# Kernel tuning notes

Measured on AMD Instinct MI355X. Metric: run time of the kernel, lower is better.

Reference implementation:

```python
import jax, jax.numpy as jnp
import numpy as np

N_NODES = 100000
N_EDGES = 1200000
IN_CH = 128
HID = 256
OUT_CH = 64
N_ETYPES = 8
N_DIFF = 1000


def setup_inputs() -> dict:
    key = jax.random.key(0)
    ks = jax.random.split(key, 20)
    s = 0.05
    inp = {
        'x': jax.random.normal(ks[0], (N_NODES, IN_CH), jnp.float32),
        'edge_index': jax.random.randint(ks[1], (2, N_EDGES), 0, N_NODES, jnp.int64),
        'edge_type': jax.random.randint(ks[2], (N_EDGES,), 0, N_ETYPES, jnp.int64),
        'diff_idx': jax.random.randint(ks[3], (N_DIFF,), 0, N_NODES, jnp.int64),
        # lin: in_ch -> hid -> out_ch
        'lin1_w': jax.random.normal(ks[4], (HID, IN_CH), jnp.float32) * s,
        'lin1_b': jnp.zeros((HID,), jnp.float32),
        'lin2_w': jax.random.normal(ks[5], (OUT_CH, HID), jnp.float32) * s,
        'lin2_b': jnp.zeros((OUT_CH,), jnp.float32),
        # GRUCell(out_ch, out_ch): gates ordered r, z, n as in torch
        'gru_w_ih': jax.random.normal(ks[6], (3 * OUT_CH, OUT_CH), jnp.float32) * s,
        'gru_w_hh': jax.random.normal(ks[7], (3 * OUT_CH, OUT_CH), jnp.float32) * s,
        'gru_b_ih': jnp.zeros((3 * OUT_CH,), jnp.float32),
        'gru_b_hh': jnp.zeros((3 * OUT_CH,), jnp.float32),
        'edge_type_weight': jax.random.normal(ks[8], (N_ETYPES,), jnp.float32),
        # fc: out_ch -> hid -> 2
        'fc1_w': jax.random.normal(ks[9], (HID, OUT_CH), jnp.float32) * s,
        'fc1_b': jnp.zeros((HID,), jnp.float32),
        'fc2_w': jax.random.normal(ks[10], (2, HID), jnp.float32) * s,
        'fc2_b': jnp.zeros((2,), jnp.float32),
        'w_imp': jnp.float32(1.0),
    }
    return inp


def _gru_cell(m, h, w_ih, w_hh, b_ih, b_hh):
    # torch GRUCell: gates [r, z, n]
    gi = m @ w_ih.T + b_ih  # [N, 3H]
    gh = h @ w_hh.T + b_hh
    gi_r, gi_z, gi_n = jnp.split(gi, 3, axis=-1)
    gh_r, gh_z, gh_n = jnp.split(gh, 3, axis=-1)
    r = jax.nn.sigmoid(gi_r + gh_r)
    z = jax.nn.sigmoid(gi_z + gh_z)
    n = jnp.tanh(gi_n + r * gh_n)
    return (1.0 - z) * n + z * h


def reference(x, edge_index, edge_type, diff_idx,
              lin1_w, lin1_b, lin2_w, lin2_b,
              gru_w_ih, gru_w_hh, gru_b_ih, gru_b_hh,
              edge_type_weight,
              fc1_w, fc1_b, fc2_w, fc2_b, w_imp):
    N = x.shape[0]
    src, dst = edge_index[0], edge_index[1]
    # input projection MLP
    h = jax.nn.relu(x @ lin1_w.T + lin1_b) @ lin2_w.T + lin2_b  # [N, OUT]
    # per-edge softplus weight (constant across iterations)
    w_e = jax.nn.softplus(edge_type_weight[edge_type])[:, None]  # [E, 1]
    # degree for mean aggregation (isolated nodes -> 0 message)
    deg = jax.ops.segment_sum(jnp.ones_like(src, dtype=h.dtype), dst, num_segments=N)
    deg = jnp.maximum(deg, 1.0)[:, None]
    for _ in range(3):
        msg = w_e * h[src]  # gather + weight, [E, OUT]
        m = jax.ops.segment_sum(msg, dst, num_segments=N) / deg  # scatter-mean
        h = _gru_cell(m, h, gru_w_ih, gru_w_hh, gru_b_ih, gru_b_hh)
    # importance-weighted global pooling
    w_pos = jax.nn.softplus(w_imp)
    alpha = jnp.ones((N, 1), h.dtype).at[diff_idx].set(1.0 + w_pos)
    pooled = (alpha * h).sum(axis=0, keepdims=True) / alpha.sum()  # [1, OUT]
    out = jax.nn.relu(pooled @ fc1_w.T + fc1_b) @ fc2_w.T + fc2_b  # [1, 2]
    return jax.nn.log_softmax(out, axis=1)
```

## Files before the change

kernel.cpp:

```cpp
#include <hip/hip_runtime.h>
#include <math.h>

#define NN 100000
#define NE 1200000
#define NDIFF 1000
#define CAP 48
#define SLICE 2048
#define NQ 200
#define SUBN 500
#define QCAPB 32
#define NSH 8
#define SQS 1024
#define NSPLAY 32
#define PSTRIDE 132

typedef short short8 __attribute__((ext_vector_type(8)));
typedef float floatx4 __attribute__((ext_vector_type(4)));
typedef float floatx2 __attribute__((ext_vector_type(2)));
typedef unsigned short ushort_t;
typedef unsigned long long ull_t;

__device__ __forceinline__ float softplusf_(float x) {
  return fmaxf(x, 0.f) + logf(1.f + __expf(-fabsf(x)));
}
__device__ __forceinline__ float sigmoidf_(float x) {
  return 1.f / (1.f + __expf(-x));
}
__device__ __forceinline__ float tanhf_fast(float x) {
  float ax = fabsf(x);
  float e = __expf(-2.f * ax);
  float t = (1.f - e) / (1.f + e);
  return x < 0.f ? -t : t;
}
__device__ __forceinline__ ushort_t f2bf(float f) {
  unsigned u = __float_as_uint(f);
  unsigned r = (u + 0x7FFFu + ((u >> 16) & 1u)) >> 16;
  return (ushort_t)r;
}
__device__ __forceinline__ float bf2f(ushort_t s) {
  return __uint_as_float(((unsigned)s) << 16);
}
__device__ __forceinline__ uint2 bf8_to_fp8x8(short8 v) {
  float f[8];
  #pragma unroll
  for (int i = 0; i < 8; ++i) f[i] = bf2f((ushort_t)v[i]);
  int a = 0, b = 0;
  a = __builtin_amdgcn_cvt_pk_fp8_f32(f[0], f[1], a, false);
  a = __builtin_amdgcn_cvt_pk_fp8_f32(f[2], f[3], a, true);
  b = __builtin_amdgcn_cvt_pk_fp8_f32(f[4], f[5], b, false);
  b = __builtin_amdgcn_cvt_pk_fp8_f32(f[6], f[7], b, true);
  uint2 r; r.x = (unsigned)a; r.y = (unsigned)b;
  return r;
}


__global__ void prep_w_kernel(const float* __restrict__ lin1_w, const float* __restrict__ lin2_w,
                              const float* __restrict__ w_ih, const float* __restrict__ w_hh,
                              const float* __restrict__ etw, const int* __restrict__ diff,
                              ushort_t* __restrict__ W1s, ushort_t* __restrict__ W2s,
                              ushort_t* __restrict__ Wcs, float* __restrict__ wtab,
                              unsigned char* __restrict__ flagb) {
  int i = blockIdx.x * 256 + threadIdx.x;
  if (i < 8) wtab[i] = softplusf_(etw[i]);
  if (i < NDIFF) flagb[diff[i]] = 1;
  if (i < 32768) {
    int fi = i >> 9, lane = (i >> 3) & 63, j = i & 7;
    int s = fi >> 4, ct = fi & 15;
    int quad = lane >> 4, l15 = lane & 15;
    int col = ct * 16 + l15, k = s * 32 + quad * 8 + j;
    W1s[i] = f2bf(lin1_w[col * 128 + k]);
  } else if (i < 49152) {
    int i2 = i - 32768;
    int fi = i2 >> 9, lane = (i2 >> 3) & 63, j = i2 & 7;
    int s = fi >> 2, ct = fi & 3;
    int quad = lane >> 4, l15 = lane & 15;
    int col = ct * 16 + l15, k = s * 32 + quad * 8 + j;
    W2s[i2] = f2bf(lin2_w[col * 256 + k]);
  } else {
    int i3 = i - 49152;
    int fi = i3 >> 9, lane = (i3 >> 3) & 63, j = i3 & 7;
    int s = fi >> 4, ct = fi & 15;
    int quad = lane >> 4, l15 = lane & 15;
    int jj = ct * 16 + l15, k = s * 32 + quad * 8 + j;
    float v;
    if (jj < 128)      v = (k < 64) ? w_ih[jj * 64 + k] : w_hh[jj * 64 + (k - 64)];
    else if (jj < 192) v = (k < 64) ? w_ih[jj * 64 + k] : 0.f;
    else               v = (k < 64) ? 0.f : w_hh[(jj - 64) * 64 + (k - 64)];
    Wcs[i3] = f2bf(v);
  }
}


__launch_bounds__(256)
__global__ void bin_kernel(const int* __restrict__ src, const int* __restrict__ dst,
                           const int* __restrict__ etype,
                           unsigned* __restrict__ gtail, ull_t* __restrict__ staging) {
  __shared__ uint2 bin[NQ][QCAPB];
  __shared__ unsigned lcur[NQ];
  int t = threadIdx.x;
  int shard = blockIdx.x & 7;
  for (int i = t; i < NQ; i += 256) lcur[i] = 0;
  __syncthreads();
  int base = blockIdx.x * SLICE;

  uint2 rec[8];
  int qq[8];
  unsigned idx[8];
  #pragma unroll
  for (int it = 0; it < 8; ++it) {
    int e = base + it * 256 + t;
    qq[it] = -1;
    if (e < NE) {
      int d = __builtin_nontemporal_load(&dst[e]);
      int s = __builtin_nontemporal_load(&src[e]);
      int tv = __builtin_nontemporal_load(&etype[e]);
      rec[it].x = (unsigned)(s | (tv << 17));
      rec[it].y = (unsigned)d;
      int q = d / SUBN;
      qq[it] = q;
      unsigned i = atomicAdd(&lcur[q], 1u);
      idx[it] = i;
      if (i < QCAPB) bin[q][i] = rec[it];
    }
  }
  __syncthreads();
  if (t < NQ) {
    unsigned c = min(lcur[t], (unsigned)QCAPB);
    if (c) {
      unsigned gb = atomicAdd(&gtail[(t * NSH + shard) * 16], c);
      ull_t* qst = staging + (size_t)(t * NSH + shard) * SQS + gb;
      const uint2* b = bin[t];
      for (unsigned i = 0; i < c; ++i)
        qst[i] = ((ull_t)b[i].y << 32) | (ull_t)b[i].x;
    }
  }
  #pragma unroll
  for (int it = 0; it < 8; ++it) {
    if (qq[it] >= 0 && idx[it] >= QCAPB) {
      unsigned gb = atomicAdd(&gtail[(qq[it] * NSH + shard) * 16], 1u);
      staging[(size_t)(qq[it] * NSH + shard) * SQS + gb] =
          ((ull_t)rec[it].y << 32) | (ull_t)rec[it].x;
    }
  }
}

__launch_bounds__(512)
__global__ void scatter_kernel(const ull_t* __restrict__ staging,
                               const unsigned* __restrict__ gtail,
                               unsigned* __restrict__ cpack, int* __restrict__ csr) {
  __shared__ int cnt[SUBN];
  int t = threadIdx.x;
  int q = blockIdx.x;
  int n0 = q * SUBN;
  for (int i = t; i < SUBN; i += 512) cnt[i] = 0;
  __syncthreads();

  #pragma unroll 1
  for (int sh = 0; sh < NSH; ++sh) {
    unsigned n = gtail[(q * NSH + sh) * 16];
    const ull_t* st = staging + (size_t)(q * NSH + sh) * SQS;
    for (unsigned i = t; i < n; i += 512) {
      ull_t r = st[i];
      int d = (int)(r >> 32);
      int rank = atomicAdd(&cnt[d - n0], 1);
      csr[d * CAP + rank] = (int)(unsigned)r;
    }
  }
  __syncthreads();

  if (t < SUBN / 4) {
    unsigned w = (unsigned)cnt[t * 4] | ((unsigned)cnt[t * 4 + 1] << 8) |
                 ((unsigned)cnt[t * 4 + 2] << 16) | ((unsigned)cnt[t * 4 + 3] << 24);
    cpack[(n0 >> 2) + t] = w;
  }
}


__launch_bounds__(256)
__global__ void mlp_kernel(const float* __restrict__ x,
                           const ushort_t* __restrict__ W1s, const float* __restrict__ b1,
                           const ushort_t* __restrict__ W2s, const float* __restrict__ b2,
                           ushort_t* __restrict__ mh, unsigned char* __restrict__ h8) {
  __shared__ ushort_t S[64 * 264];
  int t = threadIdx.x;
  int wv = t >> 6, lane = t & 63;
  int quad = lane >> 4, l15 = lane & 15;
  int nb = blockIdx.x * 64;

  #pragma unroll
  for (int it = 0; it < 8; ++it) {
    int f = it * 256 + t;
    int row = f >> 5, off4 = f & 31;
    int grow = min(nb + row, NN - 1);
    float4 v = *(const float4*)&x[(size_t)grow * 128 + off4 * 4];
    union { uint2 d; ushort_t u[4]; } pk;
    pk.u[0] = f2bf(v.x); pk.u[1] = f2bf(v.y); pk.u[2] = f2bf(v.z); pk.u[3] = f2bf(v.w);
    *(uint2*)&S[row * 136 + off4 * 4] = pk.d;
  }
  __syncthreads();

  floatx4 acc1[4][4];
  #pragma unroll
  for (int rt = 0; rt < 4; ++rt)
    #pragma unroll
    for (int c = 0; c < 4; ++c) acc1[rt][c] = (floatx4)0.f;

  #pragma unroll
  for (int s = 0; s < 4; ++s) {
    short8 av[4];
    #pragma unroll
    for (int rt = 0; rt < 4; ++rt)
      av[rt] = *(const short8*)&S[(rt * 16 + l15) * 136 + s * 32 + quad * 8];
    #pragma unroll
    for (int c = 0; c < 4; ++c) {
      short8 bv = *(const short8*)&W1s[((s * 16 + wv * 4 + c) * 64 + lane) * 8];
      #pragma unroll
      for (int rt = 0; rt < 4; ++rt)
        acc1[rt][c] = __builtin_amdgcn_mfma_f32_16x16x32_bf16(av[rt], bv, acc1[rt][c], 0, 0, 0);
    }
  }
  __syncthreads();

  #pragma unroll
  for (int c = 0; c < 4; ++c) {
    int col = (wv * 4 + c) * 16 + l15;
    float bb = b1[col];
    #pragma unroll
    for (int rt = 0; rt < 4; ++rt)
      #pragma unroll
      for (int reg = 0; reg < 4; ++reg)
        S[(rt * 16 + quad * 4 + reg) * 264 + col] = f2bf(fmaxf(acc1[rt][c][reg] + bb, 0.f));
  }
  __syncthreads();

  floatx4 acc2[4];
  #pragma unroll
  for (int c = 0; c < 4; ++c) acc2[c] = (floatx4)0.f;
  #pragma unroll
  for (int s = 0; s < 8; ++s) {
    short8 av = *(const short8*)&S[(wv * 16 + l15) * 264 + s * 32 + quad * 8];
    #pragma unroll
    for (int c = 0; c < 4; ++c) {
      short8 bv = *(const short8*)&W2s[((s * 4 + c) * 64 + lane) * 8];
      acc2[c] = __builtin_amdgcn_mfma_f32_16x16x32_bf16(av, bv, acc2[c], 0, 0, 0);
    }
  }
  __syncthreads();

  #pragma unroll
  for (int c = 0; c < 4; ++c) {
    int col = c * 16 + l15;
    float bb = b2[c * 16 + l15];
    #pragma unroll
    for (int reg = 0; reg < 4; ++reg)
      S[(wv * 16 + quad * 4 + reg) * 72 + col] = f2bf(acc2[c][reg] + bb);
  }
  __syncthreads();

  #pragma unroll
  for (int it = 0; it < 2; ++it) {
    int idx = it * 256 + t;
    int row = idx >> 3, ch = idx & 7;
    int node = nb + row;
    if (node < NN) {
      short8 v = *(const short8*)&S[row * 72 + ch * 8];
      *(short8*)&mh[(size_t)node * 64 + ch * 8] = v;
      *(uint2*)&h8[(size_t)node * 64 + ch * 8] = bf8_to_fp8x8(v);
    }
  }
}


template <bool LAST>
__launch_bounds__(256, 8)
__global__ void agru_kernel(const ushort_t* __restrict__ mhin,
                            const unsigned char* __restrict__ h8in,
                            const unsigned* __restrict__ cpack,
                            const int* __restrict__ csr, const float* __restrict__ wtab,
                            const ushort_t* __restrict__ Wcs,
                            const float* __restrict__ b_ih, const float* __restrict__ b_hh,
                            ushort_t* __restrict__ mhout, unsigned char* __restrict__ h8out,
                            const unsigned char* __restrict__ flagb,
                            float* __restrict__ pooled) {
  __shared__ ushort_t As[32 * 136];
  __shared__ ushort_t Os[32 * 72];
  __shared__ float wt[16];
  __shared__ float red[132];
  int t = threadIdx.x;
  int nb = blockIdx.x * 32;
  if (t < 16) wt[t] = (t < 8) ? wtab[t] : 0.f;
  if (LAST) { for (int i = t; i < 132; i += 256) red[i] = 0.f; }
  __syncthreads();

  int g8 = t >> 3, lane8 = t & 7;
  int node = nb + g8;

  short8 hreg = *(const short8*)&mhin[(size_t)node * 64 + lane8 * 8];

  int deg = (cpack[node >> 2] >> ((node & 3) * 8)) & 255;
  int s = node * CAP;
  float f0 = 0.f, f1 = 0.f, f2 = 0.f, f3 = 0.f;
  float f4 = 0.f, f5 = 0.f, f6 = 0.f, f7 = 0.f;
  for (int p = 0; p < deg; p += 8) {
    int k[8];
    uint2 v[8];
    #pragma unroll
    for (int i = 0; i < 8; ++i) {
      int q = p + i;
      k[i] = (q < deg) ? __builtin_nontemporal_load(&csr[s + q]) : (8 << 17);
    }
    #pragma unroll
    for (int i = 0; i < 8; ++i)
      v[i] = *(const uint2*)&h8in[(size_t)(k[i] & 0x1FFFF) * 64 + lane8 * 8];
    #pragma unroll
    for (int i = 0; i < 8; ++i) {
      float w = wt[k[i] >> 17];
      floatx2 xlo = __builtin_amdgcn_cvt_pk_f32_fp8((int)v[i].x, false);
      floatx2 xhi = __builtin_amdgcn_cvt_pk_f32_fp8((int)v[i].x, true);
      floatx2 ylo = __builtin_amdgcn_cvt_pk_f32_fp8((int)v[i].y, false);
      floatx2 yhi = __builtin_amdgcn_cvt_pk_f32_fp8((int)v[i].y, true);
      f0 += w * xlo[0]; f1 += w * xlo[1]; f2 += w * xhi[0]; f3 += w * xhi[1];
      f4 += w * ylo[0]; f5 += w * ylo[1]; f6 += w * yhi[0]; f7 += w * yhi[1];
    }
  }
  {
    float invd = 1.f / fmaxf((float)deg, 1.f);
    short8 pk;
    pk[0] = (short)f2bf(f0 * invd); pk[1] = (short)f2bf(f1 * invd);
    pk[2] = (short)f2bf(f2 * invd); pk[3] = (short)f2bf(f3 * invd);
    pk[4] = (short)f2bf(f4 * invd); pk[5] = (short)f2bf(f5 * invd);
    pk[6] = (short)f2bf(f6 * invd); pk[7] = (short)f2bf(f7 * invd);
    *(short8*)&As[g8 * 136 + lane8 * 8] = pk;
    *(short8*)&As[g8 * 136 + 64 + lane8 * 8] = hreg;
  }
  __syncthreads();

  int wv = t >> 6, lane = t & 63;
  int quad = lane >> 4, l15 = lane & 15;

  floatx4 acc[2][4];
  #pragma unroll
  for (int rt = 0; rt < 2; ++rt)
    #pragma unroll
    for (int g = 0; g < 4; ++g) acc[rt][g] = (floatx4)0.f;

  #pragma unroll
  for (int s4 = 0; s4 < 4; ++s4) {
    short8 av[2];
    #pragma unroll
    for (int rt = 0; rt < 2; ++rt)
      av[rt] = *(const short8*)&As[(rt * 16 + l15) * 136 + s4 * 32 + quad * 8];
    #pragma unroll
    for (int g = 0; g < 4; ++g) {
      short8 bv = *(const short8*)&Wcs[((s4 * 16 + g * 4 + wv) * 64 + lane) * 8];
      #pragma unroll
      for (int rt = 0; rt < 2; ++rt)
        acc[rt][g] = __builtin_amdgcn_mfma_f32_16x16x32_bf16(av[rt], bv, acc[rt][g], 0, 0, 0);
    }
  }

  int j = wv * 16 + l15;
  float bir = b_ih[j] + b_hh[j];
  float biz = b_ih[64 + j] + b_hh[64 + j];
  float bin_ = b_ih[128 + j];
  float bhn = b_hh[128 + j];

  if (!LAST) {
    #pragma unroll
    for (int rt = 0; rt < 2; ++rt) {
      #pragma unroll
      for (int reg = 0; reg < 4; ++reg) {
        int lrow = rt * 16 + quad * 4 + reg;
        float r = sigmoidf_(acc[rt][0][reg] + bir);
        float z = sigmoidf_(acc[rt][1][reg] + biz);
        float n = tanhf_fast(acc[rt][2][reg] + bin_ + r * (acc[rt][3][reg] + bhn));
        float hp = bf2f(As[lrow * 136 + 64 + j]);
        Os[lrow * 72 + j] = f2bf((1.f - z) * n + z * hp);
      }
    }
    __syncthreads();
    short8 vo = *(const short8*)&Os[g8 * 72 + lane8 * 8];
    *(short8*)&mhout[(size_t)node * 64 + lane8 * 8] = vo;
    *(uint2*)&h8out[(size_t)node * 64 + lane8 * 8] = bf8_to_fp8x8(vo);
  } else {
    float psum = 0.f, fsum = 0.f;
    #pragma unroll
    for (int rt = 0; rt < 2; ++rt) {
      #pragma unroll
      for (int reg = 0; reg < 4; ++reg) {
        int lrow = rt * 16 + quad * 4 + reg;
        float r = sigmoidf_(acc[rt][0][reg] + bir);
        float z = sigmoidf_(acc[rt][1][reg] + biz);
        float n = tanhf_fast(acc[rt][2][reg] + bin_ + r * (acc[rt][3][reg] + bhn));
        float hp = bf2f(As[lrow * 136 + 64 + j]);
        float hn = (1.f - z) * n + z * hp;
        psum += hn;
        if (flagb[nb + lrow]) fsum += hn;
      }
    }
    atomicAdd(&red[j], psum);
    atomicAdd(&red[64 + j], fsum);
    if (t < 32) { if (flagb[nb + t]) atomicAdd(&red[128], 1.f); }
    __syncthreads();
    if (t < 129) atomicAdd(&pooled[(blockIdx.x & (NSPLAY - 1)) * PSTRIDE + t], red[t]);
  }
}


__global__ void final_kernel(const float* __restrict__ pooled,
                             const float* __restrict__ fc1_w, const float* __restrict__ fc1_b,
                             const float* __restrict__ fc2_w, const float* __restrict__ fc2_b,
                             const float* __restrict__ w_imp, float* __restrict__ out) {
  __shared__ float p[64];
  __shared__ float hid[256];
  __shared__ float o[2];
  __shared__ float cnt_s;
  int t = threadIdx.x;
  float wpos = softplusf_(w_imp[0]);
  float b = 0.f, f = 0.f;
  if (t < 64) {
    #pragma unroll 4
    for (int k = 0; k < NSPLAY; ++k) {
      b += pooled[k * PSTRIDE + t];
      f += pooled[k * PSTRIDE + 64 + t];
    }
  }
  if (t == 64) {
    float c = 0.f;
    for (int k = 0; k < NSPLAY; ++k) c += pooled[k * PSTRIDE + 128];
    cnt_s = c;
  }
  __syncthreads();
  if (t < 64) {
    float den = (float)NN + wpos * cnt_s;
    p[t] = (b + wpos * f) / den;
  }
  __syncthreads();
  {
    float a = 0.f;
    for (int k = 0; k < 64; ++k) a += p[k] * fc1_w[t * 64 + k];
    hid[t] = fmaxf(a + fc1_b[t], 0.f);
  }
  __syncthreads();
  if (t < 2) {
    float a = 0.f;
    for (int k = 0; k < 256; ++k) a += hid[k] * fc2_w[t * 256 + k];
    o[t] = a + fc2_b[t];
  }
  __syncthreads();
  if (t == 0) {
    float mx = fmaxf(o[0], o[1]);
    float lse = mx + logf(__expf(o[0] - mx) + __expf(o[1] - mx));
    out[0] = o[0] - lse;
    out[1] = o[1] - lse;
  }
}


extern "C" void kernel_launch(void* const* d_in, const int* in_sizes, int n_in,
                              void* d_out, int out_size, void* d_ws, size_t ws_size,
                              hipStream_t stream) {
  const float* x        = (const float*)d_in[0];
  const int*   ei       = (const int*)d_in[1];
  const int*   etype    = (const int*)d_in[2];
  const int*   diff_idx = (const int*)d_in[3];
  const float* lin1_w   = (const float*)d_in[4];
  const float* lin1_b   = (const float*)d_in[5];
  const float* lin2_w   = (const float*)d_in[6];
  const float* lin2_b   = (const float*)d_in[7];
  const float* gru_w_ih = (const float*)d_in[8];
  const float* gru_w_hh = (const float*)d_in[9];
  const float* gru_b_ih = (const float*)d_in[10];
  const float* gru_b_hh = (const float*)d_in[11];
  const float* etw      = (const float*)d_in[12];
  const float* fc1_w    = (const float*)d_in[13];
  const float* fc1_b    = (const float*)d_in[14];
  const float* fc2_w    = (const float*)d_in[15];
  const float* fc2_b    = (const float*)d_in[16];
  const float* w_imp    = (const float*)d_in[17];
  float* out = (float*)d_out;

  char* ws = (char*)d_ws;
  size_t off = 0;
  auto alloc = [&](size_t bytes) -> void* {
    void* p = ws + off;
    off += (bytes + 255) & ~(size_t)255;
    return p;
  };
  ushort_t* mh0   = (ushort_t*)alloc((size_t)NN * 64 * 2);
  ushort_t* mh1   = (ushort_t*)alloc((size_t)NN * 64 * 2);
  unsigned char* h8a = (unsigned char*)alloc((size_t)NN * 64);
  unsigned char* h8b = (unsigned char*)alloc((size_t)NN * 64);
  int*   csr      = (int*)  alloc((size_t)NN * CAP * 4);
  ull_t* staging  = (ull_t*)alloc((size_t)NQ * NSH * SQS * 8);
  ushort_t* W1s   = (ushort_t*)alloc(128 * 256 * 2);
  ushort_t* W2s   = (ushort_t*)alloc(256 * 64 * 2);
  ushort_t* Wcs   = (ushort_t*)alloc(128 * 256 * 2);
  float* wtab     = (float*)alloc(8 * 4);
  const size_t gtb = (size_t)NQ * NSH * 16 * 4;
  const size_t plb = (size_t)NSPLAY * PSTRIDE * 4;
  char* zbase     = (char*)alloc(gtb + (size_t)NN + NN + plb);
  unsigned* gtail = (unsigned*)zbase;
  unsigned* cpack = (unsigned*)(zbase + gtb);
  unsigned char* flagb = (unsigned char*)(zbase + gtb + NN);
  float* pooled   = (float*)(zbase + gtb + NN + NN);
  const size_t zbytes = gtb + (size_t)NN + NN + plb;

  const int ngemm = (NN + 63) / 64;
  const int nagru = NN / 32;
  const int nbin  = (NE + SLICE - 1) / SLICE;

  hipMemsetAsync(zbase, 0, zbytes, stream);
  prep_w_kernel<<<320, 256, 0, stream>>>(lin1_w, lin2_w, gru_w_ih, gru_w_hh, etw, diff_idx,
                                         W1s, W2s, Wcs, wtab, flagb);
  bin_kernel<<<nbin, 256, 0, stream>>>(ei, ei + NE, etype, gtail, staging);
  scatter_kernel<<<NQ, 512, 0, stream>>>(staging, gtail, cpack, csr);
  mlp_kernel<<<ngemm, 256, 0, stream>>>(x, W1s, lin1_b, W2s, lin2_b, mh0, h8a);

  agru_kernel<false><<<nagru, 256, 0, stream>>>(mh0, h8a, cpack, csr, wtab, Wcs,
                                                gru_b_ih, gru_b_hh, mh1, h8b, flagb, pooled);
  agru_kernel<false><<<nagru, 256, 0, stream>>>(mh1, h8b, cpack, csr, wtab, Wcs,
                                                gru_b_ih, gru_b_hh, mh0, h8a, flagb, pooled);
  agru_kernel<true><<<nagru, 256, 0, stream>>>(mh0, h8a, cpack, csr, wtab, Wcs,
                                               gru_b_ih, gru_b_hh, mh1, h8b, flagb, pooled);

  final_kernel<<<1, 256, 0, stream>>>(pooled, fc1_w, fc1_b, fc2_w, fc2_b, w_imp, out);
}
```

Before: 322.6 us.

## Fuse edge binning with input MLP and pack staging records into 32 bits

Merges the edge-binning kernel and the input-projection MLP kernel into one launch, with block ranges split by blockIdx, so the two independent phases can run concurrently and one launch is saved. Staging records shrink from 64-bit to 32-bit by storing the node's local offset within its partition instead of the full destination, which halves staging traffic. The aggregation loop now reads CSR indices as 16-byte vectors, 12 per iteration instead of 8 scalar loads, with extra padding on the CSR allocation. Risks are shared-memory and occupancy changes in the fused kernel and reads past the degree in the vector loads.

```diff
diff --git a/kernel.cpp b/kernel.cpp
--- a/kernel.cpp
+++ b/kernel.cpp
@@ -13,10 +13,13 @@
 #define SQS 1024
 #define NSPLAY 32
 #define PSTRIDE 132
+#define NGEMM 1563
+#define NBIN 586
 
 typedef short short8 __attribute__((ext_vector_type(8)));
 typedef float floatx4 __attribute__((ext_vector_type(4)));
 typedef float floatx2 __attribute__((ext_vector_type(2)));
+typedef int intx4 __attribute__((ext_vector_type(4)));
 typedef unsigned short ushort_t;
 typedef unsigned long long ull_t;
 
@@ -92,60 +95,155 @@
 
 
 __launch_bounds__(256)
-__global__ void bin_kernel(const int* __restrict__ src, const int* __restrict__ dst,
-                           const int* __restrict__ etype,
-                           unsigned* __restrict__ gtail, ull_t* __restrict__ staging) {
-  __shared__ uint2 bin[NQ][QCAPB];
-  __shared__ unsigned lcur[NQ];
+__global__ void binmlp_kernel(const float* __restrict__ x,
+                              const ushort_t* __restrict__ W1s, const float* __restrict__ b1,
+                              const ushort_t* __restrict__ W2s, const float* __restrict__ b2,
+                              ushort_t* __restrict__ mh, unsigned char* __restrict__ h8,
+                              const int* __restrict__ src, const int* __restrict__ dst,
+                              const int* __restrict__ etype,
+                              unsigned* __restrict__ gtail, unsigned* __restrict__ staging) {
+  __shared__ __align__(16) char U[33792];
   int t = threadIdx.x;
-  int shard = blockIdx.x & 7;
-  for (int i = t; i < NQ; i += 256) lcur[i] = 0;
-  __syncthreads();
-  int base = blockIdx.x * SLICE;
-
-  uint2 rec[8];
-  int qq[8];
-  unsigned idx[8];
-  #pragma unroll
-  for (int it = 0; it < 8; ++it) {
-    int e = base + it * 256 + t;
-    qq[it] = -1;
-    if (e < NE) {
-      int d = __builtin_nontemporal_load(&dst[e]);
-      int s = __builtin_nontemporal_load(&src[e]);
-      int tv = __builtin_nontemporal_load(&etype[e]);
-      rec[it].x = (unsigned)(s | (tv << 17));
-      rec[it].y = (unsigned)d;
-      int q = d / SUBN;
-      qq[it] = q;
-      unsigned i = atomicAdd(&lcur[q], 1u);
-      idx[it] = i;
-      if (i < QCAPB) bin[q][i] = rec[it];
-    }
-  }
-  __syncthreads();
-  if (t < NQ) {
-    unsigned c = min(lcur[t], (unsigned)QCAPB);
-    if (c) {
-      unsigned gb = atomicAdd(&gtail[(t * NSH + shard) * 16], c);
-      ull_t* qst = staging + (size_t)(t * NSH + shard) * SQS + gb;
-      const uint2* b = bin[t];
-      for (unsigned i = 0; i < c; ++i)
-        qst[i] = ((ull_t)b[i].y << 32) | (ull_t)b[i].x;
-    }
-  }
-  #pragma unroll
-  for (int it = 0; it < 8; ++it) {
-    if (qq[it] >= 0 && idx[it] >= QCAPB) {
-      unsigned gb = atomicAdd(&gtail[(qq[it] * NSH + shard) * 16], 1u);
-      staging[(size_t)(qq[it] * NSH + shard) * SQS + gb] =
-          ((ull_t)rec[it].y << 32) | (ull_t)rec[it].x;
-    }
-  }
-}
+
+  if (blockIdx.x < NGEMM) {
+    ushort_t* S = (ushort_t*)U;
+    int wv = t >> 6, lane = t & 63;
+    int quad = lane >> 4, l15 = lane & 15;
+    int nb = blockIdx.x * 64;
+
+    #pragma unroll
+    for (int it = 0; it < 8; ++it) {
+      int f = it * 256 + t;
+      int row = f >> 5, off4 = f & 31;
+      int grow = min(nb + row, NN - 1);
+      float4 v = *(const float4*)&x[(size_t)grow * 128 + off4 * 4];
+      union { uint2 d; ushort_t u[4]; } pk;
+      pk.u[0] = f2bf(v.x); pk.u[1] = f2bf(v.y); pk.u[2] = f2bf(v.z); pk.u[3] = f2bf(v.w);
+      *(uint2*)&S[row * 136 + off4 * 4] = pk.d;
+    }
+    __syncthreads();
+
+    floatx4 acc1[4][4];
+    #pragma unroll
+    for (int rt = 0; rt < 4; ++rt)
+      #pragma unroll
+      for (int c = 0; c < 4; ++c) acc1[rt][c] = (floatx4)0.f;
+
+    #pragma unroll
+    for (int s = 0; s < 4; ++s) {
+      short8 av[4];
+      #pragma unroll
+      for (int rt = 0; rt < 4; ++rt)
+        av[rt] = *(const short8*)&S[(rt * 16 + l15) * 136 + s * 32 + quad * 8];
+      #pragma unroll
+      for (int c = 0; c < 4; ++c) {
+        short8 bv = *(const short8*)&W1s[((s * 16 + wv * 4 + c) * 64 + lane) * 8];
+        #pragma unroll
+        for (int rt = 0; rt < 4; ++rt)
+          acc1[rt][c] = __builtin_amdgcn_mfma_f32_16x16x32_bf16(av[rt], bv, acc1[rt][c], 0, 0, 0);
+      }
+    }
+    __syncthreads();
+
+    #pragma unroll
+    for (int c = 0; c < 4; ++c) {
+      int col = (wv * 4 + c) * 16 + l15;
+      float bb = b1[col];
+      #pragma unroll
+      for (int rt = 0; rt < 4; ++rt)
+        #pragma unroll
+        for (int reg = 0; reg < 4; ++reg)
+          S[(rt * 16 + quad * 4 + reg) * 264 + col] = f2bf(fmaxf(acc1[rt][c][reg] + bb, 0.f));
+    }
+    __syncthreads();
+
+    floatx4 acc2[4];
+    #pragma unroll
+    for (int c = 0; c < 4; ++c) acc2[c] = (floatx4)0.f;
+    #pragma unroll
+    for (int s = 0; s < 8; ++s) {
+      short8 av = *(const short8*)&S[(wv * 16 + l15) * 264 + s * 32 + quad * 8];
+      #pragma unroll
+      for (int c = 0; c < 4; ++c) {
+        short8 bv = *(const short8*)&W2s[((s * 4 + c) * 64 + lane) * 8];
+        acc2[c] = __builtin_amdgcn_mfma_f32_16x16x32_bf16(av, bv, acc2[c], 0, 0, 0);
+      }
+    }
+    __syncthreads();
+
+    #pragma unroll
+    for (int c = 0; c < 4; ++c) {
+      int col = c * 16 + l15;
+      float bb = b2[c * 16 + l15];
+      #pragma unroll
+      for (int reg = 0; reg < 4; ++reg)
+        S[(wv * 16 + quad * 4 + reg) * 72 + col] = f2bf(acc2[c][reg] + bb);
+    }
+    __syncthreads();
+
+    #pragma unroll
+    for (int it = 0; it < 2; ++it) {
+      int idx = it * 256 + t;
+      int row = idx >> 3, ch = idx & 7;
+      int node = nb + row;
+      if (node < NN) {
+        short8 v = *(const short8*)&S[row * 72 + ch * 8];
+        *(short8*)&mh[(size_t)node * 64 + ch * 8] = v;
+        *(uint2*)&h8[(size_t)node * 64 + ch * 8] = bf8_to_fp8x8(v);
+      }
+    }
+  } else {
+    unsigned (*bin)[QCAPB] = (unsigned (*)[QCAPB])U;
+    unsigned* lcur = (unsigned*)(U + NQ * QCAPB * 4);
+    int bid = blockIdx.x - NGEMM;
+    int shard = bid & 7;
+    for (int i = t; i < NQ; i += 256) lcur[i] = 0;
+    __syncthreads();
+    int base = bid * SLICE;
+
+    unsigned rec[8];
+    int qq[8];
+    unsigned idx[8];
+    #pragma unroll
+    for (int it = 0; it < 8; ++it) {
+      int e = base + it * 256 + t;
+      qq[it] = -1;
+      if (e < NE) {
+        int d = __builtin_nontemporal_load(&dst[e]);
+        int s = __builtin_nontemporal_load(&src[e]);
+        int tv = __builtin_nontemporal_load(&etype[e]);
+        int q = d / SUBN;
+        int local = d - q * SUBN;
+        rec[it] = ((unsigned)local << 20) | (unsigned)(s | (tv << 17));
+        qq[it] = q;
+        unsigned i = atomicAdd(&lcur[q], 1u);
+        idx[it] = i;
+        if (i < QCAPB) bin[q][i] = rec[it];
+      }
+    }
+    __syncthreads();
+    if (t < NQ) {
+      unsigned c = min(lcur[t], (unsigned)QCAPB);
+      if (c) {
+        unsigned gb = atomicAdd(&gtail[(t * NSH + shard) * 16], c);
+        unsigned* qst = staging + (size_t)(t * NSH + shard) * SQS + gb;
+        const unsigned* b = bin[t];
+        for (unsigned i = 0; i < c; ++i) qst[i] = b[i];
+      }
+    }
+    #pragma unroll
+    for (int it = 0; it < 8; ++it) {
+      if (qq[it] >= 0 && idx[it] >= QCAPB) {
+        unsigned gb = atomicAdd(&gtail[(qq[it] * NSH + shard) * 16], 1u);
+        staging[(size_t)(qq[it] * NSH + shard) * SQS + gb] = rec[it];
+      }
+    }
+  }
+}
+
 
 __launch_bounds__(512)
-__global__ void scatter_kernel(const ull_t* __restrict__ staging,
+__global__ void scatter_kernel(const unsigned* __restrict__ staging,
                                const unsigned* __restrict__ gtail,
                                unsigned* __restrict__ cpack, int* __restrict__ csr) {
   __shared__ int cnt[SUBN];
@@ -158,12 +256,12 @@
   #pragma unroll 1
   for (int sh = 0; sh < NSH; ++sh) {
     unsigned n = gtail[(q * NSH + sh) * 16];
-    const ull_t* st = staging + (size_t)(q * NSH + sh) * SQS;
+    const unsigned* st = staging + (size_t)(q * NSH + sh) * SQS;
     for (unsigned i = t; i < n; i += 512) {
-      ull_t r = st[i];
-      int d = (int)(r >> 32);
-      int rank = atomicAdd(&cnt[d - n0], 1);
-      csr[d * CAP + rank] = (int)(unsigned)r;
+      unsigned r = st[i];
+      int local = r >> 20;
+      int rank = atomicAdd(&cnt[local], 1);
+      csr[(n0 + local) * CAP + rank] = (int)(r & 0xFFFFF);
     }
   }
   __syncthreads();
@@ -172,101 +270,6 @@
     unsigned w = (unsigned)cnt[t * 4] | ((unsigned)cnt[t * 4 + 1] << 8) |
                  ((unsigned)cnt[t * 4 + 2] << 16) | ((unsigned)cnt[t * 4 + 3] << 24);
     cpack[(n0 >> 2) + t] = w;
-  }
-}
-
-
-__launch_bounds__(256)
-__global__ void mlp_kernel(const float* __restrict__ x,
-                           const ushort_t* __restrict__ W1s, const float* __restrict__ b1,
-                           const ushort_t* __restrict__ W2s, const float* __restrict__ b2,
-                           ushort_t* __restrict__ mh, unsigned char* __restrict__ h8) {
-  __shared__ ushort_t S[64 * 264];
-  int t = threadIdx.x;
-  int wv = t >> 6, lane = t & 63;
-  int quad = lane >> 4, l15 = lane & 15;
-  int nb = blockIdx.x * 64;
-
-  #pragma unroll
-  for (int it = 0; it < 8; ++it) {
-    int f = it * 256 + t;
-    int row = f >> 5, off4 = f & 31;
-    int grow = min(nb + row, NN - 1);
-    float4 v = *(const float4*)&x[(size_t)grow * 128 + off4 * 4];
-    union { uint2 d; ushort_t u[4]; } pk;
-    pk.u[0] = f2bf(v.x); pk.u[1] = f2bf(v.y); pk.u[2] = f2bf(v.z); pk.u[3] = f2bf(v.w);
-    *(uint2*)&S[row * 136 + off4 * 4] = pk.d;
-  }
-  __syncthreads();
-
-  floatx4 acc1[4][4];
-  #pragma unroll
-  for (int rt = 0; rt < 4; ++rt)
-    #pragma unroll
-    for (int c = 0; c < 4; ++c) acc1[rt][c] = (floatx4)0.f;
-
-  #pragma unroll
-  for (int s = 0; s < 4; ++s) {
-    short8 av[4];
-    #pragma unroll
-    for (int rt = 0; rt < 4; ++rt)
-      av[rt] = *(const short8*)&S[(rt * 16 + l15) * 136 + s * 32 + quad * 8];
-    #pragma unroll
-    for (int c = 0; c < 4; ++c) {
-      short8 bv = *(const short8*)&W1s[((s * 16 + wv * 4 + c) * 64 + lane) * 8];
-      #pragma unroll
-      for (int rt = 0; rt < 4; ++rt)
-        acc1[rt][c] = __builtin_amdgcn_mfma_f32_16x16x32_bf16(av[rt], bv, acc1[rt][c], 0, 0, 0);
-    }
-  }
-  __syncthreads();
-
-  #pragma unroll
-  for (int c = 0; c < 4; ++c) {
-    int col = (wv * 4 + c) * 16 + l15;
-    float bb = b1[col];
-    #pragma unroll
-    for (int rt = 0; rt < 4; ++rt)
-      #pragma unroll
-      for (int reg = 0; reg < 4; ++reg)
-        S[(rt * 16 + quad * 4 + reg) * 264 + col] = f2bf(fmaxf(acc1[rt][c][reg] + bb, 0.f));
-  }
-  __syncthreads();
-
-  floatx4 acc2[4];
-  #pragma unroll
-  for (int c = 0; c < 4; ++c) acc2[c] = (floatx4)0.f;
-  #pragma unroll
-  for (int s = 0; s < 8; ++s) {
-    short8 av = *(const short8*)&S[(wv * 16 + l15) * 264 + s * 32 + quad * 8];
-    #pragma unroll
-    for (int c = 0; c < 4; ++c) {
-      short8 bv = *(const short8*)&W2s[((s * 4 + c) * 64 + lane) * 8];
-      acc2[c] = __builtin_amdgcn_mfma_f32_16x16x32_bf16(av, bv, acc2[c], 0, 0, 0);
-    }
-  }
-  __syncthreads();
-
-  #pragma unroll
-  for (int c = 0; c < 4; ++c) {
-    int col = c * 16 + l15;
-    float bb = b2[c * 16 + l15];
-    #pragma unroll
-    for (int reg = 0; reg < 4; ++reg)
-      S[(wv * 16 + quad * 4 + reg) * 72 + col] = f2bf(acc2[c][reg] + bb);
-  }
-  __syncthreads();
-
-  #pragma unroll
-  for (int it = 0; it < 2; ++it) {
-    int idx = it * 256 + t;
-    int row = idx >> 3, ch = idx & 7;
-    int node = nb + row;
-    if (node < NN) {
-      short8 v = *(const short8*)&S[row * 72 + ch * 8];
-      *(short8*)&mh[(size_t)node * 64 + ch * 8] = v;
-      *(uint2*)&h8[(size_t)node * 64 + ch * 8] = bf8_to_fp8x8(v);
-    }
   }
 }
 
@@ -298,22 +301,29 @@
   short8 hreg = *(const short8*)&mhin[(size_t)node * 64 + lane8 * 8];
 
   int deg = (cpack[node >> 2] >> ((node & 3) * 8)) & 255;
-  int s = node * CAP;
+  const intx4* crow = (const intx4*)(csr + (size_t)node * CAP);
   float f0 = 0.f, f1 = 0.f, f2 = 0.f, f3 = 0.f;
   float f4 = 0.f, f5 = 0.f, f6 = 0.f, f7 = 0.f;
-  for (int p = 0; p < deg; p += 8) {
-    int k[8];
-    uint2 v[8];
-    #pragma unroll
-    for (int i = 0; i < 8; ++i) {
-      int q = p + i;
-      k[i] = (q < deg) ? __builtin_nontemporal_load(&csr[s + q]) : (8 << 17);
-    }
-    #pragma unroll
-    for (int i = 0; i < 8; ++i)
+  for (int p = 0; p < deg; p += 12) {
+    intx4 k4[3];
+    #pragma unroll
+    for (int c = 0; c < 3; ++c)
+      k4[c] = __builtin_nontemporal_load(&crow[(p >> 2) + c]);
+    int k[12];
+    #pragma unroll
+    for (int c = 0; c < 3; ++c) {
+      k[c * 4 + 0] = k4[c][0]; k[c * 4 + 1] = k4[c][1];
+      k[c * 4 + 2] = k4[c][2]; k[c * 4 + 3] = k4[c][3];
+    }
+    #pragma unroll
+    for (int i = 0; i < 12; ++i)
+      if (p + i >= deg) k[i] = (8 << 17);
+    uint2 v[12];
+    #pragma unroll
+    for (int i = 0; i < 12; ++i)
       v[i] = *(const uint2*)&h8in[(size_t)(k[i] & 0x1FFFF) * 64 + lane8 * 8];
     #pragma unroll
-    for (int i = 0; i < 8; ++i) {
+    for (int i = 0; i < 12; ++i) {
       float w = wt[k[i] >> 17];
       floatx2 xlo = __builtin_amdgcn_cvt_pk_f32_fp8((int)v[i].x, false);
       floatx2 xhi = __builtin_amdgcn_cvt_pk_f32_fp8((int)v[i].x, true);
@@ -491,8 +501,8 @@
   ushort_t* mh1   = (ushort_t*)alloc((size_t)NN * 64 * 2);
   unsigned char* h8a = (unsigned char*)alloc((size_t)NN * 64);
   unsigned char* h8b = (unsigned char*)alloc((size_t)NN * 64);
-  int*   csr      = (int*)  alloc((size_t)NN * CAP * 4);
-  ull_t* staging  = (ull_t*)alloc((size_t)NQ * NSH * SQS * 8);
+  int*   csr      = (int*)  alloc((size_t)NN * CAP * 4 + 64);
+  unsigned* staging = (unsigned*)alloc((size_t)NQ * NSH * SQS * 4);
   ushort_t* W1s   = (ushort_t*)alloc(128 * 256 * 2);
   ushort_t* W2s   = (ushort_t*)alloc(256 * 64 * 2);
   ushort_t* Wcs   = (ushort_t*)alloc(128 * 256 * 2);
@@ -506,16 +516,14 @@
   float* pooled   = (float*)(zbase + gtb + NN + NN);
   const size_t zbytes = gtb + (size_t)NN + NN + plb;
 
-  const int ngemm = (NN + 63) / 64;
   const int nagru = NN / 32;
-  const int nbin  = (NE + SLICE - 1) / SLICE;
-
-  hipMemsetAsync(zbase, 0, zbytes, stream);
+
+  (void)hipMemsetAsync(zbase, 0, zbytes, stream);
   prep_w_kernel<<<320, 256, 0, stream>>>(lin1_w, lin2_w, gru_w_ih, gru_w_hh, etw, diff_idx,
                                          W1s, W2s, Wcs, wtab, flagb);
-  bin_kernel<<<nbin, 256, 0, stream>>>(ei, ei + NE, etype, gtail, staging);
+  binmlp_kernel<<<NGEMM + NBIN, 256, 0, stream>>>(x, W1s, lin1_b, W2s, lin2_b, mh0, h8a,
+                                                  ei, ei + NE, etype, gtail, staging);
   scatter_kernel<<<NQ, 512, 0, stream>>>(staging, gtail, cpack, csr);
-  mlp_kernel<<<ngemm, 256, 0, stream>>>(x, W1s, lin1_b, W2s, lin2_b, mh0, h8a);
 
   agru_kernel<false><<<nagru, 256, 0, stream>>>(mh0, h8a, cpack, csr, wtab, Wcs,
                                                 gru_b_ih, gru_b_hh, mh1, h8b, flagb, pooled);
```

Result: faster. 293.5 us (-9.0%).
